# Optimization experiments

Hardware: AMD Instinct MI355X
Metric: run time of the kernel (lower is better)

Reference implementation:

```python
import jax, jax.numpy as jnp
import numpy as np

N_NODES = 170
SEQ = 12
BATCH = 32
D_MODEL = 120
N_HEADS = 8
FF_DIM = 2048
K_CHEB = 3  # K=2 -> K+1 = 3 polynomial orders
LN_EPS = 1e-5


def _layer_norm(x, g, b):
    m = jnp.mean(x, -1, keepdims=True)
    v = jnp.mean((x - m) ** 2, -1, keepdims=True)
    return (x - m) * jax.lax.rsqrt(v + LN_EPS) * g + b


def _graph_learn(adj, beta, w1, w2, cw, cb):
    # learned antisymmetric adjacency + 1x1-conv gating + double sym-normalization
    n = adj.shape[0]
    eps = 0.5 / n
    new = jax.nn.relu(w1 @ w2.T - w2 @ w1.T + jnp.diag(beta))
    gate = jax.nn.sigmoid(cw[0] * new + cw[1] * adj + cb)  # Conv2d(2,1,1) == weighted sum
    a = gate * new + (1.0 - gate) * adj
    d = jax.lax.rsqrt(jnp.sum(a, 1))
    a = jax.nn.relu(d[:, None] * a * d[None, :] - eps)
    d = jax.lax.rsqrt(jnp.sum(a, 1))
    return d[:, None] * a * d[None, :]


def _cheb_conv(x2d, graph, w, b):
    # x2d: (B*T, N, C); graph: (N, N); w: (K, C, O); b: (O,)
    n = graph.shape[0]
    d = jax.lax.rsqrt(jnp.sum(graph, -1))
    eye = jnp.eye(n, dtype=x2d.dtype)
    L = eye - d[:, None] * graph * d[None, :]
    Ts = [eye, L]
    for _ in range(w.shape[0] - 2):
        Ts.append(2.0 * (L @ Ts[-1]) - Ts[-2])
    T = jnp.stack(Ts)  # (K, N, N)
    h = jnp.einsum('knm,bmc->kbnc', T, x2d)
    return jnp.einsum('kbnc,kco->bno', h, w) + b


def setup_inputs() -> dict:
    key = jax.random.key(0)
    ks = jax.random.split(key, 16)
    D, F = D_MODEL, FF_DIM
    kaiming = 1.0 / np.sqrt(D)  # kaiming_uniform(a=sqrt(5)) bound for fan_in=D
    xavier = float(np.sqrt(2.0 / (D + D)))
    return {
        'x': jax.random.normal(ks[0], (BATCH, SEQ, N_NODES, D), jnp.float32),
        'adj': jax.random.uniform(ks[1], (N_NODES, N_NODES), jnp.float32),
        # GraphLearn params, stacked for Q/K/V branches (leading dim 3)
        'gl_beta': jax.random.uniform(ks[2], (3, N_NODES), jnp.float32),
        'gl_w1': jax.random.uniform(ks[3], (3, N_NODES, D), jnp.float32, -kaiming, kaiming),
        'gl_w2': jax.random.uniform(ks[4], (3, N_NODES, D), jnp.float32, -kaiming, kaiming),
        'gl_cw': jax.random.normal(ks[5], (3, 2), jnp.float32) * 0.5,
        'gl_cb': jnp.zeros((3,), jnp.float32),
        # ChebConv params per branch
        'cheb_w': jax.random.normal(ks[6], (3, K_CHEB, D, D), jnp.float32) * xavier,
        'cheb_b': jnp.zeros((3, D), jnp.float32),
        # output projection + FFN + layernorms
        'out_w': jax.random.normal(ks[7], (D, D), jnp.float32) / np.sqrt(D),
        'out_b': jnp.zeros((D,), jnp.float32),
        'ff_w1': jax.random.normal(ks[8], (D, F), jnp.float32) / np.sqrt(D),
        'ff_b1': jnp.zeros((F,), jnp.float32),
        'ff_w2': jax.random.normal(ks[9], (F, D), jnp.float32) / np.sqrt(F),
        'ff_b2': jnp.zeros((D,), jnp.float32),
        'ln1_g': jnp.ones((D,), jnp.float32),
        'ln1_b': jnp.zeros((D,), jnp.float32),
        'ln2_g': jnp.ones((D,), jnp.float32),
        'ln2_b': jnp.zeros((D,), jnp.float32),
    }


def reference(x, adj, gl_beta, gl_w1, gl_w2, gl_cw, gl_cb, cheb_w, cheb_b,
              out_w, out_b, ff_w1, ff_b1, ff_w2, ff_b2, ln1_g, ln1_b, ln2_g, ln2_b):
    B, T, N, D = x.shape
    H = N_HEADS
    hd = D // H
    x2d = x.reshape(B * T, N, D)
    qkv = []
    for i in range(3):  # Q, K, V branches (structurally distinct params)
        g = _graph_learn(adj, gl_beta[i], gl_w1[i], gl_w2[i], gl_cw[i], gl_cb[i])
        g = jax.lax.stop_gradient(g)  # torch code does graph.clone().detach()
        h = jax.nn.relu(_cheb_conv(x2d, g, cheb_w[i], cheb_b[i]))
        qkv.append(h.reshape(B, T, N, D))
    q, k, v = qkv

    def to_heads(t):  # (B,T,N,D) -> (B,N,T,H,hd)
        return t.transpose(0, 2, 1, 3).reshape(B, N, T, H, hd)
    q, k, v = to_heads(q), to_heads(k), to_heads(v)
    scores = jnp.einsum('bnqhd,bnkhd->bnhqk', q, k) / (hd ** 0.5)
    attn = jax.nn.softmax(scores, axis=-1)
    o = jnp.einsum('bnhqk,bnkhd->bnqhd', attn, v).reshape(B, N, T, D)
    o = o @ out_w + out_b  # (B,N,T,D)
    out = _layer_norm(x + o.transpose(0, 2, 1, 3), ln1_g, ln1_b)  # residual in (B,T,N,D)
    ff = jax.nn.relu(out @ ff_w1 + ff_b1) @ ff_w2 + ff_b2
    out = _layer_norm(out + ff, ln2_g, ln2_b)
    return out
```

## Files before the change

### kernel.cpp

```cpp
#include <hip/hip_runtime.h>
#include <cstddef>
#include <cstdint>

#define N_NODES 170
#define SEQ 12
#define BATCH 32
#define DM 120
#define BT (BATCH*SEQ)
#define ROWS (BT*N_NODES)
#define FF 2048

typedef short short8 __attribute__((ext_vector_type(8)));
typedef float f32x4 __attribute__((ext_vector_type(4)));

static constexpr size_t OFF_A    = 0;
static constexpr size_t OFF_G    = 86704;
static constexpr size_t OFF_A2   = 173408;
static constexpr size_t OFF_L    = 260112;
static constexpr size_t OFF_RS1  = 307824;
static constexpr size_t OFF_RS2  = 308336;
static constexpr size_t OFF_RS3  = 308848;
static constexpr size_t OFF_XT   = 309360;
static constexpr size_t OFF_XNM  = OFF_XT  + 4325376;
static constexpr size_t OFF_HK   = OFF_XNM + 4177920;
static constexpr size_t OFF_HV   = OFF_HK  + 4177920;
static constexpr size_t OFF_YNM  = OFF_HV  + 4177920;
static constexpr size_t OFF_BC   = OFF_YNM + 3*8355840;
static constexpr size_t OFF_W1T  = OFF_BC  + 73728;
static constexpr size_t OFF_W2R  = OFF_W1T + 131072;
static constexpr size_t OFF_OWT  = OFF_W2R + 131072;
static constexpr size_t OFF_HQ   = OFF_XT;
static constexpr size_t OFF_ONM  = OFF_YNM;
static constexpr size_t OFF_LN1  = OFF_ONM + 4177920;
static constexpr size_t OFF_LN1B = OFF_LN1 + 7833600;

static constexpr size_t YNM_BR_STRIDE = 16711680;

__device__ __forceinline__ unsigned short f2bf(float f) {
    unsigned int u = __float_as_uint(f);
    unsigned int r = (u + 0x7fffu + ((u >> 16) & 1u)) >> 16;
    return (unsigned short)r;
}
__device__ __forceinline__ float bf2f(unsigned short h) {
    return __uint_as_float(((unsigned int)h) << 16);
}
__device__ __forceinline__ void gld16(const void* g, void* l) {
    __builtin_amdgcn_global_load_lds(
        (const __attribute__((address_space(1))) void*)g,
        (__attribute__((address_space(3))) void*)l, 16, 0, 0);
}
__device__ __forceinline__ uint4 pack8(const unsigned short v[8]) {
    uint4 q;
    q.x = (unsigned)v[0] | ((unsigned)v[1] << 16);
    q.y = (unsigned)v[2] | ((unsigned)v[3] << 16);
    q.z = (unsigned)v[4] | ((unsigned)v[5] << 16);
    q.w = (unsigned)v[6] | ((unsigned)v[7] << 16);
    return q;
}

__global__ __launch_bounds__(256)
void k_gl1(const float* __restrict__ adj, const float* __restrict__ beta,
           const float* __restrict__ w1, const float* __restrict__ w2,
           const float* __restrict__ cw, const float* __restrict__ cb,
           float* __restrict__ a_out, float* __restrict__ rs_out) {
    int i  = blockIdx.x;
    int br = blockIdx.y;
    __shared__ float w1r[DM], w2r[DM];
    __shared__ float red[256];
    int tid = threadIdx.x;
    const float* w1b = w1 + (size_t)br * N_NODES * DM;
    const float* w2b = w2 + (size_t)br * N_NODES * DM;
    if (tid < DM) {
        w1r[tid] = w1b[(size_t)i * DM + tid];
        w2r[tid] = w2b[(size_t)i * DM + tid];
    }
    __syncthreads();
    float aval = 0.f;
    if (tid < N_NODES) {
        int j = tid;
        const float4* w1j = (const float4*)(w1b + (size_t)j * DM);
        const float4* w2j = (const float4*)(w2b + (size_t)j * DM);
        float s1 = 0.f, s2 = 0.f;
#pragma unroll 6
        for (int cc = 0; cc < DM / 4; ++cc) {
            float4 u = w2j[cc];
            float4 v = w1j[cc];
            s1 += w1r[cc*4+0]*u.x + w1r[cc*4+1]*u.y + w1r[cc*4+2]*u.z + w1r[cc*4+3]*u.w;
            s2 += w2r[cc*4+0]*v.x + w2r[cc*4+1]*v.y + w2r[cc*4+2]*v.z + w2r[cc*4+3]*v.w;
        }
        float nv = s1 - s2 + (j == i ? beta[br * N_NODES + i] : 0.f);
        nv = fmaxf(nv, 0.f);
        float adjv = adj[(size_t)i * N_NODES + j];
        float z = cw[br*2+0] * nv + cw[br*2+1] * adjv + cb[br];
        float gate = 1.f / (1.f + __expf(-z));
        aval = gate * nv + (1.f - gate) * adjv;
        a_out[((size_t)br * N_NODES + i) * N_NODES + j] = aval;
    }
    red[tid] = aval;
    __syncthreads();
    for (int s = 128; s > 0; s >>= 1) {
        if (tid < s) red[tid] += red[tid + s];
        __syncthreads();
    }
    if (tid == 0) rs_out[br * N_NODES + i] = red[0];
}

__global__ __launch_bounds__(256)
void k_glnorm(const float* __restrict__ in, const float* __restrict__ rs,
              float* __restrict__ out, float* __restrict__ rs_out, int mode) {
    int i  = blockIdx.x;
    int br = blockIdx.y;
    __shared__ float red[256];
    int tid = threadIdx.x;
    float di = rsqrtf(rs[br * N_NODES + i]);
    float contrib = 0.f;
    if (tid < N_NODES) {
        float dj = rsqrtf(rs[br * N_NODES + tid]);
        float v = di * in[((size_t)br * N_NODES + i) * N_NODES + tid] * dj;
        float o;
        if (mode == 2) { o = fmaxf(v - 0.5f / 170.f, 0.f); contrib = o; }
        else           { o = v; contrib = v; }
        out[((size_t)br * N_NODES + i) * N_NODES + tid] = o;
    }
    red[tid] = contrib;
    __syncthreads();
    for (int s = 128; s > 0; s >>= 1) {
        if (tid < s) red[tid] += red[tid + s];
        __syncthreads();
    }
    if (tid == 0) rs_out[br * N_NODES + i] = red[0];
}

__global__ __launch_bounds__(192)
void k_prep_L(const float* __restrict__ g_buf, const float* __restrict__ rs3,
              unsigned short* __restrict__ Lbf) {
    int i  = blockIdx.x;
    int br = blockIdx.y;
    int j  = threadIdx.x;
    if (j >= 180) return;
    float v = 0.f;
    if (i < N_NODES && j < N_NODES) {
        float di = rsqrtf(rs3[br * N_NODES + i]);
        float dj = rsqrtf(rs3[br * N_NODES + j]);
        float gg = g_buf[((size_t)br * N_NODES + i) * N_NODES + j];
        v = (i == j ? 1.f : 0.f) - di * gg * dj;
    }
    Lbf[(size_t)br * 31808 + i * 180 + j] = f2bf(v);
}

__global__ __launch_bounds__(256)
void k_prep_x(const float* __restrict__ x, unsigned short* __restrict__ xTF,
              unsigned short* __restrict__ xnm) {
    __shared__ unsigned short LX[170 * 121 + 8];
    int bt = blockIdx.x, tid = threadIdx.x;
    const float* xb = x + (size_t)bt * N_NODES * DM;
    for (int u = tid; u < 170 * 30; u += 256) {
        int nn = u / 30, cq = u - nn * 30;
        float4 v = *(const float4*)&xb[nn * 120 + cq * 4];
        LX[nn * 121 + cq * 4 + 0] = f2bf(v.x);
        LX[nn * 121 + cq * 4 + 1] = f2bf(v.y);
        LX[nn * 121 + cq * 4 + 2] = f2bf(v.z);
        LX[nn * 121 + cq * 4 + 3] = f2bf(v.w);
    }
    __syncthreads();
    for (int u = tid; u < 128 * 22; u += 256) {
        int c = u / 22, mb = u - c * 22;
        unsigned short vals[8];
#pragma unroll
        for (int i2 = 0; i2 < 8; ++i2) {
            int m = mb * 8 + i2;
            vals[i2] = (c < 120 && m < 170) ? LX[m * 121 + c] : (unsigned short)0;
        }
        *(uint4*)&xTF[(size_t)bt * 22528 + ((size_t)mb * 128 + c) * 8] = pack8(vals);
    }
    for (int u = tid; u < 170 * 16; u += 256) {
        int nn = u >> 4, b = u & 15;
        unsigned int row = bt * 170 + nn;
        unsigned short vals[8];
#pragma unroll
        for (int i2 = 0; i2 < 8; ++i2) {
            int c = b * 8 + i2;
            vals[i2] = (c < 120) ? LX[nn * 121 + c] : (unsigned short)0;
        }
        int bs = (b & 8) | ((b & 7) ^ (row & 7));
        *(uint4*)&xnm[(size_t)row * 128 + bs * 8] = pack8(vals);
    }
}

__global__ __launch_bounds__(256)
void k_prep_weights(const float* __restrict__ ff_w1, const float* __restrict__ ff_w2,
                    const float* __restrict__ out_w, const float* __restrict__ cheb_w,
                    unsigned short* __restrict__ W1T, unsigned short* __restrict__ W2R,
                    unsigned short* __restrict__ OwT, unsigned short* __restrict__ Bc) {
    int idx = blockIdx.x * 256 + threadIdx.x;
    if (idx < 262144) {
        int o = idx >> 7, k = idx & 127;
        int b = k >> 3, ki = k & 7;
        int pos = (((b ^ (o & 7)) << 3) | ki);
        float v = (k < DM) ? ff_w1[(size_t)k * FF + o] : 0.f;
        W1T[(size_t)o * 128 + pos] = f2bf(v);
    } else if (idx < 524288) {
        int i = idx - 262144;
        int c = i >> 13;
        int o = (i >> 6) & 127;
        int j = i & 63;
        int b = j >> 3, ji = j & 7;
        int pos = (((b ^ (o & 7)) << 3) | ji);
        float v = (o < DM) ? ff_w2[(size_t)(c * 64 + j) * DM + o] : 0.f;
        W2R[((size_t)c << 13) + (o << 6) + pos] = f2bf(v);
    } else if (idx < 540672) {
        int i = idx - 524288;
        int o = i >> 7, c = i & 127;
        float v = (o < 120 && c < 120) ? out_w[(size_t)c * 120 + o] : 0.f;
        OwT[(((size_t)(c >> 3) * 128 + o) << 3) + (c & 7)] = f2bf(v);
    } else {
        int i = idx - 540672;
        int br  = i / 49152;
        int rem = i - br * 49152;
        int o   = rem / 384;
        int c   = rem - o * 384;
        float v = 0.f;
        if (o < 120) {
            int part = c >> 7, cc = c & 127;
            if (cc < 120) {
                const float* Wb = cheb_w + (size_t)br * 3 * 14400;
                if (part == 0)      v = Wb[cc * 120 + o] - Wb[2 * 14400 + cc * 120 + o];
                else if (part == 1) v = Wb[14400 + cc * 120 + o];
                else                v = 2.f * Wb[2 * 14400 + cc * 120 + o];
            }
        }
        Bc[(size_t)br * 49152 + (((size_t)(c >> 3) * 128 + o) << 3) + (c & 7)] = f2bf(v);
    }
}

#define MP 184
__global__ __launch_bounds__(256)
void k_lapply2(const unsigned short* __restrict__ xTg,
               const unsigned short* __restrict__ Lg_base,
               unsigned short* __restrict__ ynm_base) {
    __shared__ __attribute__((aligned(16))) unsigned short Llds[31744];
    __shared__ __attribute__((aligned(16))) unsigned short Y1[128 * MP];
    const int tid = threadIdx.x, w = tid >> 6, lane = tid & 63;
    const int g = lane >> 4, l15 = lane & 15;
    const int bt = blockIdx.x, br = blockIdx.y;
    const unsigned short* Asrc = xTg + (size_t)bt * 22528;
    const unsigned short* Lg   = Lg_base + (size_t)br * 31808;
    unsigned short* ynm = ynm_base + (size_t)br * YNM_BR_STRIDE;
    const char* Lgb = (const char*)Lg;
    char* Lldsb = (char*)Llds;
#pragma unroll
    for (int it = 0; it < 16; ++it) {
        int q = it * 4 + w;
        if (q * 1024 < 63360)
            gld16(Lgb + q * 1024 + lane * 16, Lldsb + q * 1024);
    }
    short8 af[2][6];
#pragma unroll
    for (int ct2 = 0; ct2 < 2; ++ct2) {
        int c = (w * 2 + ct2) * 16 + l15;
#pragma unroll
        for (int kb = 0; kb < 6; ++kb) {
            if (kb < 5) af[ct2][kb] = *(const short8*)&Asrc[(((size_t)(kb * 4 + g)) * 128 + c) * 8];
            else {
                short8 z = {};
                af[ct2][kb] = (g < 2) ? *(const short8*)&Asrc[(((size_t)(20 + g)) * 128 + c) * 8] : z;
            }
        }
    }
    __syncthreads();
    f32x4 acc[2][11];

    for (int hop = 0; hop < 2; ++hop) {
#pragma unroll
        for (int a = 0; a < 2; ++a)
#pragma unroll
            for (int b = 0; b < 11; ++b) acc[a][b] = (f32x4){0.f, 0.f, 0.f, 0.f};
#pragma unroll
        for (int kb = 0; kb < 6; ++kb) {
#pragma unroll
            for (int nt = 0; nt < 11; ++nt) {
                short8 bf;
                int rb = (nt * 16 + l15) * 180;
                if (kb < 5) bf = *(const short8*)&Llds[rb + kb * 32 + g * 8];
                else {
                    short8 z = {};
                    bf = (g < 2) ? *(const short8*)&Llds[rb + 160 + g * 8] : z;
                }
                acc[0][nt] = __builtin_amdgcn_mfma_f32_16x16x32_bf16(af[0][kb], bf, acc[0][nt], 0, 0, 0);
                acc[1][nt] = __builtin_amdgcn_mfma_f32_16x16x32_bf16(af[1][kb], bf, acc[1][nt], 0, 0, 0);
            }
        }
        const int coloff = hop * 128;
#pragma unroll
        for (int nt = 0; nt < 11; ++nt) {
            int nn = nt * 16 + l15;
#pragma unroll
            for (int ct2 = 0; ct2 < 2; ++ct2) {
                int base_c = (w * 2 + ct2) * 16 + g * 4;
                if (hop == 0) {
#pragma unroll
                    for (int r = 0; r < 4; ++r)
                        Y1[(base_c + r) * MP + nn] = f2bf(acc[ct2][nt][r]);
                }
                if (nn < 170) {
                    unsigned int row = bt * 170 + nn;
                    unsigned short u[4];
#pragma unroll
                    for (int r = 0; r < 4; ++r)
                        u[r] = (base_c + r < 120) ? f2bf(acc[ct2][nt][r]) : (unsigned short)0;
                    int bc  = coloff + base_c;
                    int blk = bc >> 3;
                    int bsw = (blk & 24) | ((blk & 7) ^ (row & 7));
                    uint2 pk;
                    pk.x = (unsigned)u[0] | ((unsigned)u[1] << 16);
                    pk.y = (unsigned)u[2] | ((unsigned)u[3] << 16);
                    *(uint2*)&ynm[(size_t)row * 256 + bsw * 8 + (bc & 7)] = pk;
                }
            }
        }
        if (hop == 0) {
            __syncthreads();
#pragma unroll
            for (int ct2 = 0; ct2 < 2; ++ct2) {
                int c = (w * 2 + ct2) * 16 + l15;
#pragma unroll
                for (int kb = 0; kb < 6; ++kb) {
                    if (kb < 5) af[ct2][kb] = *(const short8*)&Y1[c * MP + kb * 32 + g * 8];
                    else {
                        short8 z = {};
                        af[ct2][kb] = (g < 2) ? *(const short8*)&Y1[c * MP + 160 + g * 8] : z;
                    }
                }
            }
        }
    }
}

__global__ __launch_bounds__(256)
void k_combine_mfma(const unsigned short* __restrict__ xnm,
                    const unsigned short* __restrict__ ynm_base,
                    const unsigned short* __restrict__ Bc_base,
                    const float* __restrict__ bias_base,
                    unsigned short* __restrict__ h0,
                    unsigned short* __restrict__ h1,
                    unsigned short* __restrict__ h2) {
    __shared__ __attribute__((aligned(16))) unsigned short AsX[64 * 128];
    __shared__ __attribute__((aligned(16))) unsigned short AsY[64 * 256];
    const int tid = threadIdx.x, w = tid >> 6, lane = tid & 63;
    const int g = lane >> 4, l15 = lane & 15;
    const int r0 = blockIdx.x * 64;
    const int br = blockIdx.y;
    const unsigned short* ynm = ynm_base + (size_t)br * YNM_BR_STRIDE;
    const unsigned short* Bc  = Bc_base + (size_t)br * 49152;
    const float* bias = bias_base + br * DM;
    unsigned short* Hout = (br == 0) ? h0 : (br == 1) ? h1 : h2;
#pragma unroll
    for (int it = 0; it < 4; ++it) {
        int q = w * 4 + it;
        gld16(xnm + (size_t)r0 * 128 + q * 512 + lane * 8, &AsX[q * 512]);
    }
#pragma unroll
    for (int it = 0; it < 8; ++it) {
        int q = w * 8 + it;
        gld16(ynm + (size_t)r0 * 256 + q * 512 + lane * 8, &AsY[q * 512]);
    }
    __syncthreads();
    const int lr = w * 16 + l15;
    short8 af[12];
#pragma unroll
    for (int kb = 0; kb < 4; ++kb) {
        int b = kb * 4 + g;
        int bs = (b & 8) | ((b & 7) ^ (lr & 7));
        af[kb] = *(const short8*)&AsX[lr * 128 + bs * 8];
    }
#pragma unroll
    for (int kb = 4; kb < 12; ++kb) {
        int b = (kb - 4) * 4 + g;
        int bs = (b & 24) | ((b & 7) ^ (lr & 7));
        af[kb] = *(const short8*)&AsY[lr * 256 + bs * 8];
    }
    f32x4 acc[8];
#pragma unroll
    for (int c = 0; c < 8; ++c) acc[c] = (f32x4){0.f, 0.f, 0.f, 0.f};
    short8 bfA[8], bfB[8];
#pragma unroll
    for (int c = 0; c < 8; ++c)
        bfA[c] = *(const short8*)&Bc[(((size_t)g) * 128 + c * 16 + l15) * 8];
#pragma unroll
    for (int kb = 0; kb < 12; ++kb) {
        if (kb + 1 < 12) {
#pragma unroll
            for (int c = 0; c < 8; ++c) {
                short8 v = *(const short8*)&Bc[(((size_t)((kb + 1) * 4 + g)) * 128 + c * 16 + l15) * 8];
                if (kb & 1) bfA[c] = v; else bfB[c] = v;
            }
        }
#pragma unroll
        for (int c = 0; c < 8; ++c)
            acc[c] = __builtin_amdgcn_mfma_f32_16x16x32_bf16(af[kb], (kb & 1) ? bfB[c] : bfA[c], acc[c], 0, 0, 0);
    }
#pragma unroll
    for (int c = 0; c < 8; ++c) {
        int o = c * 16 + l15;
        float bv = (o < 120) ? bias[o] : 0.f;
#pragma unroll
        for (int r = 0; r < 4; ++r) {
            int row = r0 + w * 16 + g * 4 + r;
            float v = (o < 120) ? fmaxf(acc[c][r] + bv, 0.f) : 0.f;
            Hout[(size_t)row * 128 + o] = f2bf(v);
        }
    }
}

#define QP 136
__global__ __launch_bounds__(192)
void k_attn_qkv(const unsigned short* __restrict__ hq, const unsigned short* __restrict__ hk,
                const unsigned short* __restrict__ hv, unsigned short* __restrict__ onm) {
    __shared__ unsigned short qs[2][SEQ][QP], ks[2][SEQ][QP], vs[2][SEQ][QP], os[2][SEQ][QP];
    const int tid = threadIdx.x;
    const int np = blockIdx.x, b = blockIdx.y;
    for (int u = tid; u < 2 * SEQ * 16; u += 192) {
        int node = u / (SEQ * 16);
        int rem = u - node * SEQ * 16;
        int t = rem >> 4, seg = rem & 15;
        int n = np * 2 + node;
        size_t row = ((size_t)(b * SEQ + t) * N_NODES + n);
        *(uint4*)&qs[node][t][seg * 8] = *(const uint4*)&hq[row * 128 + seg * 8];
        *(uint4*)&ks[node][t][seg * 8] = *(const uint4*)&hk[row * 128 + seg * 8];
        *(uint4*)&vs[node][t][seg * 8] = *(const uint4*)&hv[row * 128 + seg * 8];
    }
    __syncthreads();
    {
        const int node = tid / 96, sub = tid % 96;
        const int h = sub & 7, tq = sub >> 3;
        float qr[15];
#pragma unroll
        for (int d = 0; d < 15; ++d) qr[d] = bf2f(qs[node][tq][h * 15 + d]);
        float sc[SEQ];
        float mx = -1e30f;
#pragma unroll
        for (int tk = 0; tk < SEQ; ++tk) {
            float s = 0.f;
#pragma unroll
            for (int d = 0; d < 15; ++d) s += qr[d] * bf2f(ks[node][tk][h * 15 + d]);
            s *= 0.25819888974716113f;
            sc[tk] = s;
            mx = fmaxf(mx, s);
        }
        float sum = 0.f;
#pragma unroll
        for (int tk = 0; tk < SEQ; ++tk) { sc[tk] = __expf(sc[tk] - mx); sum += sc[tk]; }
        float inv = 1.f / sum;
#pragma unroll
        for (int d = 0; d < 15; ++d) {
            float o = 0.f;
#pragma unroll
            for (int tk = 0; tk < SEQ; ++tk) o += sc[tk] * bf2f(vs[node][tk][h * 15 + d]);
            os[node][tq][h * 15 + d] = f2bf(o * inv);
        }
    }
    if (tid < 2 * SEQ) {
        int node = tid / SEQ, t = tid % SEQ;
#pragma unroll
        for (int j = 0; j < 8; ++j) os[node][t][120 + j] = 0;
    }
    __syncthreads();
    for (int u = tid; u < 2 * SEQ * 16; u += 192) {
        int node = u / (SEQ * 16);
        int rem = u - node * SEQ * 16;
        int t = rem >> 4, seg = rem & 15;
        int n = np * 2 + node;
        unsigned int row = (b * SEQ + t) * N_NODES + n;
        int bs = (seg & 8) | ((seg & 7) ^ (row & 7));
        *(uint4*)&onm[(size_t)row * 128 + bs * 8] = *(const uint4*)&os[node][t][seg * 8];
    }
}

__global__ __launch_bounds__(256)
void k_outproj(const unsigned short* __restrict__ onm, const unsigned short* __restrict__ OwT,
               const float* __restrict__ outb, const float* __restrict__ x,
               const float* __restrict__ g1, const float* __restrict__ be1,
               float* __restrict__ ln1, unsigned short* __restrict__ ln1bf) {
    __shared__ __attribute__((aligned(16))) unsigned short As[64 * 128];
    const int tid = threadIdx.x, w = tid >> 6, lane = tid & 63;
    const int g = lane >> 4, l15 = lane & 15;
    const int r0 = blockIdx.x * 64;
#pragma unroll
    for (int it = 0; it < 4; ++it) {
        int q = w * 4 + it;
        gld16(onm + (size_t)r0 * 128 + q * 512 + lane * 8, &As[q * 512]);
    }
    __syncthreads();
    const int lr = w * 16 + l15;
    short8 af[4];
#pragma unroll
    for (int kb = 0; kb < 4; ++kb) {
        int b = kb * 4 + g;
        int bs = (b & 8) | ((b & 7) ^ (lr & 7));
        af[kb] = *(const short8*)&As[lr * 128 + bs * 8];
    }
    f32x4 acc[8];
#pragma unroll
    for (int c = 0; c < 8; ++c) acc[c] = (f32x4){0.f, 0.f, 0.f, 0.f};
#pragma unroll
    for (int kb = 0; kb < 4; ++kb) {
#pragma unroll
        for (int c = 0; c < 8; ++c) {
            short8 bf = *(const short8*)&OwT[(((size_t)(kb * 4 + g)) * 128 + c * 16 + l15) * 8];
            acc[c] = __builtin_amdgcn_mfma_f32_16x16x32_bf16(af[kb], bf, acc[c], 0, 0, 0);
        }
    }
#pragma unroll
    for (int r = 0; r < 4; ++r) {
        int row = w * 16 + g * 4 + r;
        size_t grow = (size_t)(r0 + row);
        float vals[8];
        float s = 0.f, q = 0.f;
#pragma unroll
        for (int c = 0; c < 8; ++c) {
            int col = c * 16 + l15;
            float v = 0.f;
            if (col < DM) v = acc[c][r] + outb[col] + x[grow * DM + col];
            vals[c] = v;
            s += v; q += v * v;
        }
#pragma unroll
        for (int m = 1; m < 16; m <<= 1) {
            s += __shfl_xor(s, m);
            q += __shfl_xor(q, m);
        }
        float mean = s * (1.f / DM);
        float var  = q * (1.f / DM) - mean * mean;
        float rstd = rsqrtf(var + 1e-5f);
#pragma unroll
        for (int c = 0; c < 8; ++c) {
            int col = c * 16 + l15;
            float o = (vals[c] - mean) * rstd * ((col < DM) ? g1[col] : 0.f) + ((col < DM) ? be1[col] : 0.f);
            if (col < DM) ln1[grow * DM + col] = o;
            ln1bf[grow * 128 + col] = (col < DM) ? f2bf(o) : (unsigned short)0;
        }
    }
}

#define LDS_XW1A 0
#define LDS_W1B  8192
#define LDS_W2A  16384
#define LDS_W2B  24576
#define LDS_HS   32768
__global__ __launch_bounds__(256, 2)
void k_ffn_mfma(const unsigned short* __restrict__ Xbf,
                const float* __restrict__ ln1,
                const unsigned short* __restrict__ W1T,
                const float* __restrict__ b1,
                const unsigned short* __restrict__ W2R,
                const float* __restrict__ b2,
                const float* __restrict__ g2, const float* __restrict__ be2,
                float* __restrict__ Out) {
    __shared__ unsigned short lds[37376];
    const int tid  = threadIdx.x;
    const int w    = tid >> 6;
    const int lane = tid & 63;
    const int g    = lane >> 4;
    const int l15  = lane & 15;
    const int r0   = blockIdx.x * 64;
    {
        const unsigned short* xsrc = Xbf + (size_t)r0 * 128;
#pragma unroll
        for (int it = 0; it < 4; ++it) {
            int seg = w * 4 + it;
            gld16(xsrc + seg * 512 + lane * 8, &lds[LDS_XW1A + seg * 512]);
        }
#pragma unroll
        for (int it = 0; it < 4; ++it) {
            int seg = w * 4 + it;
            gld16(W1T + seg * 512 + lane * 8, &lds[LDS_W1B + seg * 512]);
        }
#pragma unroll
        for (int it = 0; it < 4; ++it) {
            int seg = w * 4 + it;
            gld16(W2R + seg * 512 + lane * 8, &lds[LDS_W2A + seg * 512]);
        }
    }
    __syncthreads();
    short8 xfrag[4][4];
#pragma unroll
    for (int rt = 0; rt < 4; ++rt)
#pragma unroll
        for (int kk = 0; kk < 4; ++kk)
            xfrag[rt][kk] = *(const short8*)&lds[LDS_XW1A + (rt * 16 + l15) * 128 + kk * 32 + g * 8];

    f32x4 accO[8] = {};
    const int mycolA = w * 16 + l15;
    const int myrowB = w * 16 + l15;

    for (int t = 0; t < 32; ++t) {
        __syncthreads();
        const int p = t & 1;
        if (t + 1 < 32) {
            const unsigned short* w1src = W1T + (size_t)(t + 1) * 8192;
            const unsigned short* w2src = W2R + (size_t)(t + 1) * 8192;
            unsigned short* w1dst = &lds[(p ? LDS_W1B : LDS_XW1A)];
            unsigned short* w2dst = &lds[(p ? LDS_W2A : LDS_W2B)];
#pragma unroll
            for (int it = 0; it < 4; ++it) {
                int seg = w * 4 + it;
                gld16(w1src + seg * 512 + lane * 8, w1dst + seg * 512);
                gld16(w2src + seg * 512 + lane * 8, w2dst + seg * 512);
            }
        }
        {
            const unsigned short* w1p = &lds[p ? LDS_XW1A : LDS_W1B];
            f32x4 accA[4] = {};
#pragma unroll
            for (int kk = 0; kk < 4; ++kk) {
                int b = kk * 4 + g;
                short8 bfrag = *(const short8*)&w1p[mycolA * 128 + ((b ^ (mycolA & 7)) << 3)];
#pragma unroll
                for (int rt = 0; rt < 4; ++rt)
                    accA[rt] = __builtin_amdgcn_mfma_f32_16x16x32_bf16(bfrag, xfrag[rt][kk], accA[rt], 0, 0, 0);
            }
            float4 b4 = *(const float4*)&b1[t * 64 + w * 16 + g * 4];
            float bb[4] = {b4.x, b4.y, b4.z, b4.w};
#pragma unroll
            for (int rt = 0; rt < 4; ++rt) {
                unsigned short u[4];
#pragma unroll
                for (int r = 0; r < 4; ++r)
                    u[r] = f2bf(fmaxf(accA[rt][r] + bb[r], 0.f));
                uint2 pk;
                pk.x = (unsigned)u[0] | ((unsigned)u[1] << 16);
                pk.y = (unsigned)u[2] | ((unsigned)u[3] << 16);
                *(uint2*)&lds[LDS_HS + (rt * 16 + l15) * 72 + w * 16 + g * 4] = pk;
            }
        }
        asm volatile("s_waitcnt lgkmcnt(0)" ::: "memory");
        __builtin_amdgcn_sched_barrier(0);
        __builtin_amdgcn_s_barrier();
        {
            const unsigned short* w2p = &lds[p ? LDS_W2B : LDS_W2A];
#pragma unroll
            for (int kk = 0; kk < 2; ++kk) {
                short8 hfrag = *(const short8*)&lds[LDS_HS + myrowB * 72 + kk * 32 + g * 8];
                int b = kk * 4 + g;
#pragma unroll
                for (int c = 0; c < 8; ++c) {
                    int o = c * 16 + l15;
                    short8 w2frag = *(const short8*)&w2p[(o << 6) + ((b ^ (o & 7)) << 3)];
                    accO[c] = __builtin_amdgcn_mfma_f32_16x16x32_bf16(hfrag, w2frag, accO[c], 0, 0, 0);
                }
            }
        }
    }
#pragma unroll
    for (int r = 0; r < 4; ++r) {
        int row = w * 16 + g * 4 + r;
        size_t grow = (size_t)(r0 + row);
        float vals[8];
        float s = 0.f, q = 0.f;
#pragma unroll
        for (int c = 0; c < 8; ++c) {
            int col = c * 16 + l15;
            float v = 0.f;
            if (col < DM) v = accO[c][r] + b2[col] + ln1[grow * DM + col];
            vals[c] = v;
            s += v; q += v * v;
        }
#pragma unroll
        for (int m = 1; m < 16; m <<= 1) {
            s += __shfl_xor(s, m);
            q += __shfl_xor(q, m);
        }
        float mean = s * (1.f / DM);
        float var  = q * (1.f / DM) - mean * mean;
        float rstd = rsqrtf(var + 1e-5f);
#pragma unroll
        for (int c = 0; c < 8; ++c) {
            int col = c * 16 + l15;
            if (col < DM)
                Out[grow * DM + col] = (vals[c] - mean) * rstd * g2[col] + be2[col];
        }
    }
}

extern "C" void kernel_launch(void* const* d_in, const int* in_sizes, int n_in,
                              void* d_out, int out_size, void* d_ws, size_t ws_size,
                              hipStream_t stream) {
    const float* x      = (const float*)d_in[0];
    const float* adj    = (const float*)d_in[1];
    const float* gl_beta= (const float*)d_in[2];
    const float* gl_w1  = (const float*)d_in[3];
    const float* gl_w2  = (const float*)d_in[4];
    const float* gl_cw  = (const float*)d_in[5];
    const float* gl_cb  = (const float*)d_in[6];
    const float* cheb_w = (const float*)d_in[7];
    const float* cheb_b = (const float*)d_in[8];
    const float* out_w  = (const float*)d_in[9];
    const float* out_b  = (const float*)d_in[10];
    const float* ff_w1  = (const float*)d_in[11];
    const float* ff_b1  = (const float*)d_in[12];
    const float* ff_w2  = (const float*)d_in[13];
    const float* ff_b2  = (const float*)d_in[14];
    const float* ln1_g  = (const float*)d_in[15];
    const float* ln1_b  = (const float*)d_in[16];
    const float* ln2_g  = (const float*)d_in[17];
    const float* ln2_b  = (const float*)d_in[18];

    float* ws    = (float*)d_ws;
    float* a_buf = ws + OFF_A;
    float* g_buf = ws + OFF_G;
    float* a2buf = ws + OFF_A2;
    float* rs1   = ws + OFF_RS1;
    float* rs2   = ws + OFF_RS2;
    float* rs3   = ws + OFF_RS3;
    unsigned short* L_bf = (unsigned short*)(ws + OFF_L);
    unsigned short* xT   = (unsigned short*)(ws + OFF_XT);
    unsigned short* xnm  = (unsigned short*)(ws + OFF_XNM);
    unsigned short* ynm  = (unsigned short*)(ws + OFF_YNM);
    unsigned short* Bc   = (unsigned short*)(ws + OFF_BC);
    unsigned short* hq   = (unsigned short*)(ws + OFF_HQ);
    unsigned short* hk   = (unsigned short*)(ws + OFF_HK);
    unsigned short* hv   = (unsigned short*)(ws + OFF_HV);
    unsigned short* W1T  = (unsigned short*)(ws + OFF_W1T);
    unsigned short* W2R  = (unsigned short*)(ws + OFF_W2R);
    unsigned short* OwT  = (unsigned short*)(ws + OFF_OWT);
    unsigned short* onm  = (unsigned short*)(ws + OFF_ONM);
    float*          ln1  = ws + OFF_LN1;
    unsigned short* ln1bf= (unsigned short*)(ws + OFF_LN1B);

    k_prep_weights<<<2688, 256, 0, stream>>>(ff_w1, ff_w2, out_w, cheb_w, W1T, W2R, OwT, Bc);

    k_gl1   <<<dim3(N_NODES, 3), 256, 0, stream>>>(adj, gl_beta, gl_w1, gl_w2, gl_cw, gl_cb, a_buf, rs1);
    k_glnorm<<<dim3(N_NODES, 3), 256, 0, stream>>>(a_buf, rs1, a2buf, rs2, 2);
    k_glnorm<<<dim3(N_NODES, 3), 256, 0, stream>>>(a2buf, rs2, g_buf, rs3, 3);
    k_prep_L<<<dim3(176, 3), 192, 0, stream>>>(g_buf, rs3, L_bf);

    k_prep_x<<<BT, 256, 0, stream>>>(x, xT, xnm);

    k_lapply2<<<dim3(BT, 3), 256, 0, stream>>>(xT, L_bf, ynm);

    k_combine_mfma<<<dim3(ROWS / 64, 3), 256, 0, stream>>>(xnm, ynm, Bc, cheb_b, hq, hk, hv);

    k_attn_qkv<<<dim3(N_NODES / 2, BATCH), 192, 0, stream>>>(hq, hk, hv, onm);

    k_outproj<<<ROWS / 64, 256, 0, stream>>>(onm, OwT, out_b, x, ln1_g, ln1_b, ln1, ln1bf);

    k_ffn_mfma<<<ROWS / 64, 256, 0, stream>>>(ln1bf, ln1, W1T, ff_b1, W2R, ff_b2, ln2_g, ln2_b, (float*)d_out);
}
```

Before: 446.6 us.

## Restructure FFN kernel so each wave computes its own rows, dropping mid-iteration barrier

```diff
diff --git a/kernel.cpp b/kernel.cpp
--- a/kernel.cpp
+++ b/kernel.cpp
@@ -43,6 +43,11 @@
 }
 __device__ __forceinline__ float bf2f(unsigned short h) {
     return __uint_as_float(((unsigned int)h) << 16);
+}
+__device__ __forceinline__ unsigned cvt_pk_bf16(float lo, float hi) {
+    unsigned r;
+    asm volatile("v_cvt_pk_bf16_f32 %0, %1, %2" : "=v"(r) : "v"(lo), "v"(hi));
+    return r;
 }
 __device__ __forceinline__ void gld16(const void* g, void* l) {
     __builtin_amdgcn_global_load_lds(
@@ -542,11 +547,11 @@
     }
 }
 
-#define LDS_XW1A 0
-#define LDS_W1B  8192
-#define LDS_W2A  16384
-#define LDS_W2B  24576
-#define LDS_HS   32768
+#define LDS_W1A 0
+#define LDS_W2A 8192
+#define LDS_W1B 16384
+#define LDS_W2B 24576
+#define LDS_HS  32768
 __global__ __launch_bounds__(256, 2)
 void k_ffn_mfma(const unsigned short* __restrict__ Xbf,
                 const float* __restrict__ ln1,
@@ -568,39 +573,30 @@
 #pragma unroll
         for (int it = 0; it < 4; ++it) {
             int seg = w * 4 + it;
-            gld16(xsrc + seg * 512 + lane * 8, &lds[LDS_XW1A + seg * 512]);
-        }
-#pragma unroll
-        for (int it = 0; it < 4; ++it) {
-            int seg = w * 4 + it;
-            gld16(W1T + seg * 512 + lane * 8, &lds[LDS_W1B + seg * 512]);
-        }
-#pragma unroll
-        for (int it = 0; it < 4; ++it) {
-            int seg = w * 4 + it;
+            gld16(xsrc + seg * 512 + lane * 8, &lds[LDS_W1B + seg * 512]);
+            gld16(W1T + seg * 512 + lane * 8, &lds[LDS_W1A + seg * 512]);
             gld16(W2R + seg * 512 + lane * 8, &lds[LDS_W2A + seg * 512]);
         }
     }
     __syncthreads();
-    short8 xfrag[4][4];
-#pragma unroll
-    for (int rt = 0; rt < 4; ++rt)
-#pragma unroll
-        for (int kk = 0; kk < 4; ++kk)
-            xfrag[rt][kk] = *(const short8*)&lds[LDS_XW1A + (rt * 16 + l15) * 128 + kk * 32 + g * 8];
+    short8 xfrag[4];
+#pragma unroll
+    for (int kk = 0; kk < 4; ++kk)
+        xfrag[kk] = *(const short8*)&lds[LDS_W1B + (w * 16 + l15) * 128 + kk * 32 + g * 8];
+    __syncthreads();
 
     f32x4 accO[8] = {};
-    const int mycolA = w * 16 + l15;
-    const int myrowB = w * 16 + l15;
+    unsigned short* hs = &lds[LDS_HS + (w * 16 + l15) * 72];
+    const unsigned short* hsr = &lds[LDS_HS + (w * 16 + l15) * 72];
 
     for (int t = 0; t < 32; ++t) {
-        __syncthreads();
+        if (t) __syncthreads();
         const int p = t & 1;
         if (t + 1 < 32) {
             const unsigned short* w1src = W1T + (size_t)(t + 1) * 8192;
             const unsigned short* w2src = W2R + (size_t)(t + 1) * 8192;
-            unsigned short* w1dst = &lds[(p ? LDS_W1B : LDS_XW1A)];
-            unsigned short* w2dst = &lds[(p ? LDS_W2A : LDS_W2B)];
+            unsigned short* w1dst = &lds[p ? LDS_W1A : LDS_W1B];
+            unsigned short* w2dst = &lds[p ? LDS_W2A : LDS_W2B];
 #pragma unroll
             for (int it = 0; it < 4; ++it) {
                 int seg = w * 4 + it;
@@ -608,46 +604,35 @@
                 gld16(w2src + seg * 512 + lane * 8, w2dst + seg * 512);
             }
         }
-        {
-            const unsigned short* w1p = &lds[p ? LDS_XW1A : LDS_W1B];
-            f32x4 accA[4] = {};
+        const unsigned short* w1p = &lds[p ? LDS_W1B : LDS_W1A];
+        const unsigned short* w2p = &lds[p ? LDS_W2B : LDS_W2A];
+#pragma unroll
+        for (int ct = 0; ct < 4; ++ct) {
+            f32x4 accA = {};
 #pragma unroll
             for (int kk = 0; kk < 4; ++kk) {
-                int b = kk * 4 + g;
-                short8 bfrag = *(const short8*)&w1p[mycolA * 128 + ((b ^ (mycolA & 7)) << 3)];
-#pragma unroll
-                for (int rt = 0; rt < 4; ++rt)
-                    accA[rt] = __builtin_amdgcn_mfma_f32_16x16x32_bf16(bfrag, xfrag[rt][kk], accA[rt], 0, 0, 0);
-            }
-            float4 b4 = *(const float4*)&b1[t * 64 + w * 16 + g * 4];
-            float bb[4] = {b4.x, b4.y, b4.z, b4.w};
-#pragma unroll
-            for (int rt = 0; rt < 4; ++rt) {
-                unsigned short u[4];
-#pragma unroll
-                for (int r = 0; r < 4; ++r)
-                    u[r] = f2bf(fmaxf(accA[rt][r] + bb[r], 0.f));
-                uint2 pk;
-                pk.x = (unsigned)u[0] | ((unsigned)u[1] << 16);
-                pk.y = (unsigned)u[2] | ((unsigned)u[3] << 16);
-                *(uint2*)&lds[LDS_HS + (rt * 16 + l15) * 72 + w * 16 + g * 4] = pk;
-            }
-        }
-        asm volatile("s_waitcnt lgkmcnt(0)" ::: "memory");
-        __builtin_amdgcn_sched_barrier(0);
-        __builtin_amdgcn_s_barrier();
-        {
-            const unsigned short* w2p = &lds[p ? LDS_W2B : LDS_W2A];
-#pragma unroll
-            for (int kk = 0; kk < 2; ++kk) {
-                short8 hfrag = *(const short8*)&lds[LDS_HS + myrowB * 72 + kk * 32 + g * 8];
-                int b = kk * 4 + g;
-#pragma unroll
-                for (int c = 0; c < 8; ++c) {
-                    int o = c * 16 + l15;
-                    short8 w2frag = *(const short8*)&w2p[(o << 6) + ((b ^ (o & 7)) << 3)];
-                    accO[c] = __builtin_amdgcn_mfma_f32_16x16x32_bf16(hfrag, w2frag, accO[c], 0, 0, 0);
-                }
+                short8 w1f = *(const short8*)&w1p[(ct * 16 + l15) * 128 + (((kk * 4 + g) ^ (l15 & 7)) << 3)];
+                accA = __builtin_amdgcn_mfma_f32_16x16x32_bf16(w1f, xfrag[kk], accA, 0, 0, 0);
+            }
+            float4 b4 = *(const float4*)&b1[t * 64 + ct * 16 + g * 4];
+            float h0 = fmaxf(accA[0] + b4.x, 0.f);
+            float h1 = fmaxf(accA[1] + b4.y, 0.f);
+            float h2 = fmaxf(accA[2] + b4.z, 0.f);
+            float h3 = fmaxf(accA[3] + b4.w, 0.f);
+            uint2 pk;
+            pk.x = cvt_pk_bf16(h0, h1);
+            pk.y = cvt_pk_bf16(h2, h3);
+            *(uint2*)&hs[ct * 16 + g * 4] = pk;
+        }
+#pragma unroll
+        for (int kk = 0; kk < 2; ++kk) {
+            short8 hfrag = *(const short8*)&hsr[kk * 32 + g * 8];
+            int b = kk * 4 + g;
+#pragma unroll
+            for (int c = 0; c < 8; ++c) {
+                int o = c * 16 + l15;
+                short8 w2f = *(const short8*)&w2p[(o << 6) + ((b ^ (o & 7)) << 3)];
+                accO[c] = __builtin_amdgcn_mfma_f32_16x16x32_bf16(hfrag, w2f, accO[c], 0, 0, 0);
             }
         }
     }
```

After: 476.3 us. +6.7%, slower.
